# Optimization experiments

Hardware: AMD Instinct MI355X
Metric: run time of the kernel (lower is better)

Reference implementation:

```python
import jax, jax.numpy as jnp
import numpy as np

DEPTH = 2
DIM = 256
MLP = 1024
B = 2
N = 2048


def setup_inputs() -> dict:
    key = jax.random.key(0)
    ks = jax.random.split(key, 6)
    s = 0.02
    d = DIM
    f32 = jnp.float32
    return {
        "x": jax.random.normal(ks[0], (B, N, d), f32),
        "ln1_g": jnp.ones((DEPTH, d), f32),
        "ln1_b": jnp.zeros((DEPTH, d), f32),
        "Wqkv": (jax.random.normal(ks[1], (DEPTH, d, 3 * d), f32) * s),
        "bqkv": jnp.zeros((DEPTH, 3 * d), f32),
        "Wo": (jax.random.normal(ks[2], (DEPTH, d, d), f32) * s),
        "bo": jnp.zeros((DEPTH, d), f32),
        "ln2_g": jnp.ones((DEPTH, d), f32),
        "ln2_b": jnp.zeros((DEPTH, d), f32),
        "W1": (jax.random.normal(ks[3], (DEPTH, d, MLP), f32) * s),
        "b1": jnp.zeros((DEPTH, MLP), f32),
        "W2": (jax.random.normal(ks[4], (DEPTH, MLP, d), f32) * s),
        "b2": jnp.zeros((DEPTH, d), f32),
        "heads": 8,
    }


def _ln(x, g, b, eps=1e-5):
    m = x.mean(-1, keepdims=True)
    v = ((x - m) ** 2).mean(-1, keepdims=True)
    return (x - m) * jax.lax.rsqrt(v + eps) * g + b


def reference(x, ln1_g, ln1_b, Wqkv, bqkv, Wo, bo, ln2_g, ln2_b, W1, b1, W2, b2, heads):
    b, n, dim = x.shape
    hd = dim // heads
    scale = hd ** -0.5
    depth = Wqkv.shape[0]
    out = x
    # NOTE: faithful to original: `x` is never updated inside the loop,
    # so only the last layer's output is returned.
    for i in range(depth):
        y = _ln(x, ln1_g[i], ln1_b[i])
        qkv = y @ Wqkv[i] + bqkv[i]                      # [b,n,3*dim]
        qkv = qkv.reshape(b, n, 3, heads, hd)
        q, k, v = jnp.moveaxis(qkv, 2, 0)                # each [b,n,h,hd]
        q = q.transpose(0, 2, 1, 3)                      # [b,h,n,hd]
        k = k.transpose(0, 2, 1, 3)
        v = v.transpose(0, 2, 1, 3)
        dots = jnp.einsum('bhid,bhjd->bhij', q, k) * scale
        attn = jax.nn.softmax(dots, axis=-1)
        o = jnp.einsum('bhij,bhjd->bhid', attn, v)       # [b,h,n,hd]
        o = o.transpose(0, 2, 1, 3).reshape(b, n, dim)
        o = o @ Wo[i] + bo[i]
        a = o + x                                        # attn residual
        z = _ln(a, ln2_g[i], ln2_b[i])
        m = jax.nn.gelu(z @ W1[i] + b1[i], approximate=False) @ W2[i] + b2[i]
        out = m + a                                      # mlp residual
    return out
```

## Files before the change

kernel.cpp:

```cpp
#include <hip/hip_runtime.h>
#include <hip/hip_bf16.h>
#include <math.h>

#define DEPTHC 2
#define DIMD   256
#define MLPD   1024
#define BB     2
#define NN     2048
#define HH     8
#define HD     32
#define ROWS   (BB * NN)

typedef __attribute__((ext_vector_type(8))) short bf16x8;
typedef __attribute__((ext_vector_type(4))) float f32x4;

__device__ __forceinline__ short f2bf(float x) {
    union { float f; unsigned u; } c; c.f = x;
    unsigned u = c.u + (0x7fffu + ((c.u >> 16) & 1u));
    return (short)(u >> 16);
}
__device__ __forceinline__ float bf2f(short s) {
    union { unsigned u; float f; } c; c.u = ((unsigned)(unsigned short)s) << 16;
    return c.f;
}

__global__ __launch_bounds__(256) void prep(
    const float* __restrict__ Wqkv, const float* __restrict__ Wo,
    const float* __restrict__ W1,   const float* __restrict__ W2,
    short* __restrict__ WqkvF, short* __restrict__ WoF,
    short* __restrict__ W1F,   short* __restrict__ W2F,
    const float* __restrict__ x, const float* __restrict__ g,
    const float* __restrict__ be, short* __restrict__ y)
{
    __shared__ short Ts[128][72];

    if (blockIdx.x >= 96) {
        const int wave = threadIdx.x >> 6;
        const int lane = threadIdx.x & 63;
        const int row  = (blockIdx.x - 96) * 4 + wave;
        const int c    = lane * 4;

        const float4 v = *(const float4*)&x[(size_t)row * DIMD + c];
        float s  = v.x + v.y + v.z + v.w;
        float sq = v.x * v.x + v.y * v.y + v.z * v.z + v.w * v.w;
#pragma unroll
        for (int off = 32; off > 0; off >>= 1) {
            s  += __shfl_down(s,  off, 64);
            sq += __shfl_down(sq, off, 64);
        }
        s  = __shfl(s,  0, 64);
        sq = __shfl(sq, 0, 64);

        const float mean = s * (1.f / DIMD);
        const float var  = sq * (1.f / DIMD) - mean * mean;
        const float rstd = rsqrtf(var + 1e-5f);

        const float4 gg = *(const float4*)&g[c];
        const float4 bb = *(const float4*)&be[c];
        short4 ov;
        ov.x = f2bf((v.x - mean) * rstd * gg.x + bb.x);
        ov.y = f2bf((v.y - mean) * rstd * gg.y + bb.y);
        ov.z = f2bf((v.z - mean) * rstd * gg.z + bb.z);
        ov.w = f2bf((v.w - mean) * rstd * gg.w + bb.w);
        *(short4*)&y[(size_t)row * DIMD + c] = ov;
        return;
    }

    int blk = blockIdx.x;
    const float* W; short* WF; int K, N;
    if (blk < 24)      {           W = Wqkv; WF = WqkvF; K = 256;  N = 768;  }
    else if (blk < 32) { blk -= 24; W = Wo;   WF = WoF;   K = 256;  N = 256;  }
    else if (blk < 64) { blk -= 32; W = W1;   WF = W1F;   K = 256;  N = 1024; }
    else               { blk -= 64; W = W2;   WF = W2F;   K = 1024; N = 256;  }
    const int nkc = K >> 7;
    const int bx  = blk / nkc;
    const int kc  = blk % nkc;
    const int n0  = bx * 64;
    const int k0  = kc * 128;

    const int nc  = threadIdx.x & 63;
    const int kr0 = threadIdx.x >> 6;
#pragma unroll
    for (int i = 0; i < 32; ++i) {
        const int kr = kr0 + i * 4;
        Ts[kr][nc] = f2bf(W[(size_t)(k0 + kr) * N + n0 + nc]);
    }
    __syncthreads();

    short* out = WF + ((size_t)bx * nkc + kc) * 8192;
#pragma unroll
    for (int i = 0; i < 4; ++i) {
        const int u    = threadIdx.x + i * 256;
        const int l16  = u & 15;
        const int quad = (u >> 4) & 3;
        const int nt   = (u >> 6) & 3;
        const int ks   = (u >> 8) & 3;
        const int n    = nt * 16 + l16;
        const int kk   = (ks * 4 + quad) * 8;
        bf16x8 v;
#pragma unroll
        for (int j = 0; j < 8; ++j) v[j] = Ts[kk + j][n];
        *(bf16x8*)&out[(size_t)u * 8] = v;
    }
}

template <int K, bool GELU, bool RES, bool OBF, bool VTG>
__global__ __launch_bounds__(256) void gemm_ks(
    const short* __restrict__ A, const short* __restrict__ WF,
    const float* __restrict__ bias, const float* __restrict__ R,
    void* __restrict__ Cv, int N, short* __restrict__ vtg)
{
    __shared__ short smem[4][4096];

    const int tid  = threadIdx.x;
    const int w    = tid >> 6;
    const int lane = tid & 63;
    const int quad = lane >> 4;
    const int l16  = lane & 15;
    const int n0   = blockIdx.x * 64;
    const int m0   = blockIdx.y * 64;
    constexpr int NKC   = K / 128;
    constexpr int SLICE = K / 4;
    constexpr int NHC   = SLICE / 64;

    const short* wfb  = WF + (size_t)blockIdx.x * NKC * 8192;
    const short* arow = A + (size_t)(m0 + l16) * K + quad * 8;
    short* reg = smem[w];

    f32x4 acc[4][4] = {};

#pragma unroll
    for (int hc = 0; hc < NHC; ++hc) {
        const int kbase = w * SLICE + hc * 64;
        const short* src = wfb +
            ((size_t)(kbase >> 7) * 1024 + (size_t)((kbase >> 6) & 1) * 512) * 8;
#pragma unroll
        for (int i = 0; i < 8; ++i)
            *(bf16x8*)&reg[(i * 64 + lane) * 8] =
                *(const bf16x8*)&src[(size_t)(i * 64 + lane) * 8];

#pragma unroll
        for (int ksl = 0; ksl < 2; ++ksl) {
            const int kk = kbase + ksl * 32;
            bf16x8 af[4];
#pragma unroll
            for (int mt = 0; mt < 4; ++mt)
                af[mt] = *(const bf16x8*)(arow + (size_t)mt * 16 * K + kk);
#pragma unroll
            for (int nt = 0; nt < 4; ++nt) {
                const bf16x8 bf = *(const bf16x8*)
                    &reg[(((ksl * 4 + nt) * 4 + quad) * 16 + l16) * 8];
#pragma unroll
                for (int mt = 0; mt < 4; ++mt)
                    acc[mt][nt] = __builtin_amdgcn_mfma_f32_16x16x32_bf16(
                        af[mt], bf, acc[mt][nt], 0, 0, 0);
            }
        }
    }

#pragma unroll
    for (int p = 0; p < 2; ++p) {
        __syncthreads();
#pragma unroll
        for (int mtl = 0; mtl < 2; ++mtl)
#pragma unroll
            for (int nt = 0; nt < 4; ++nt)
                *(f32x4*)&smem[w][((mtl * 4 + nt) * 64 + lane) * 8] = acc[2 * p + mtl][nt];
        __syncthreads();
        if ((w >> 1) == p) {
            const int mtl = w & 1;
            const int mt  = 2 * p + mtl;
#pragma unroll
            for (int nt = 0; nt < 4; ++nt) {
                const int idx = ((mtl * 4 + nt) * 64 + lane) * 8;
                const f32x4 s0 = *(const f32x4*)&smem[0][idx];
                const f32x4 s1 = *(const f32x4*)&smem[1][idx];
                const f32x4 s2 = *(const f32x4*)&smem[2][idx];
                const f32x4 s3 = *(const f32x4*)&smem[3][idx];
                const f32x4 s  = (s0 + s1) + (s2 + s3);
                const int col  = n0 + nt * 16 + l16;
                const float bb = bias[col];
#pragma unroll
                for (int r = 0; r < 4; ++r) {
                    const int row = m0 + mt * 16 + quad * 4 + r;
                    float v = s[r] + bb;
                    if (RES)  v += R[(size_t)row * N + col];
                    if (GELU) v = 0.5f * v * (1.f + erff(v * 0.70710678118f));
                    const short bv = f2bf(v);
                    if (OBF) ((short*)Cv)[(size_t)row * N + col] = bv;
                    else     ((float*)Cv)[(size_t)row * N + col] = v;
                    if (VTG && n0 >= 2 * DIMD) {
                        const int vc = col - 2 * DIMD;
                        const int b  = row >> 11;
                        const int q  = row & (NN - 1);
                        const int h  = vc >> 5;
                        const int d  = vc & 31;
                        vtg[((size_t)(b * HH + h) * HD + d) * NN + q] = bv;
                    }
                }
            }
        }
    }
}

__global__ __launch_bounds__(256) void ln_kernel(
    const float* __restrict__ x, const float* __restrict__ g,
    const float* __restrict__ bta, short* __restrict__ y)
{
    const int wave = threadIdx.x >> 6;
    const int lane = threadIdx.x & 63;
    const int row  = blockIdx.x * 4 + wave;
    const int c    = lane * 4;

    const float4 v = *(const float4*)&x[(size_t)row * DIMD + c];
    float s  = v.x + v.y + v.z + v.w;
    float sq = v.x * v.x + v.y * v.y + v.z * v.z + v.w * v.w;
#pragma unroll
    for (int off = 32; off > 0; off >>= 1) {
        s  += __shfl_down(s,  off, 64);
        sq += __shfl_down(sq, off, 64);
    }
    s  = __shfl(s,  0, 64);
    sq = __shfl(sq, 0, 64);

    const float mean = s * (1.f / DIMD);
    const float var  = sq * (1.f / DIMD) - mean * mean;
    const float rstd = rsqrtf(var + 1e-5f);

    const float4 gg = *(const float4*)&g[c];
    const float4 bb = *(const float4*)&bta[c];
    short4 ov;
    ov.x = f2bf((v.x - mean) * rstd * gg.x + bb.x);
    ov.y = f2bf((v.y - mean) * rstd * gg.y + bb.y);
    ov.z = f2bf((v.z - mean) * rstd * gg.z + bb.z);
    ov.w = f2bf((v.w - mean) * rstd * gg.w + bb.w);
    *(short4*)&y[(size_t)row * DIMD + c] = ov;
}

__global__ __launch_bounds__(256) void attn_mfma(
    const short* __restrict__ qkv, const short* __restrict__ vtg,
    short* __restrict__ o)
{
    __shared__ __align__(16) short Ks2[2][64][40];
    __shared__ __align__(16) short Vs2[2][32][72];
    __shared__ __align__(16) short Ps[4][16][72];

    const int tid  = threadIdx.x;
    const int w    = tid >> 6;
    const int lane = tid & 63;
    const int quad = lane >> 4;
    const int l16  = lane & 15;
    const int qw    = w & 1;
    const int kside = w >> 1;
    const int bh   = blockIdx.y;
    const int b    = bh >> 3;
    const int h    = bh & 7;
    const int q0   = blockIdx.x * 32 + qw * 16;

    const float scale = 0.17677669529663689f;
    const float shift = 11.090354888959125f;
    const short* base = qkv + (size_t)b * NN * (3 * DIMD);

    const bf16x8 qfrag =
        *(const bf16x8*)(base + (size_t)(q0 + l16) * (3 * DIMD) + h * HD + quad * 8);

    const int side = tid >> 7;
    const int st   = tid & 127;
    const int kr   = st >> 1;
    const int kd   = (st & 1) * 16;
    const int vd   = st >> 2;
    const int vk0  = (st & 3) * 16;

    const short* kgp = base + (size_t)(side * 1024 + kr) * (3 * DIMD)
                       + DIMD + h * HD + kd;
    const short* vgp = vtg + ((size_t)bh * HD + vd) * NN + side * 1024 + vk0;

    f32x4 oacc0 = {0.f, 0.f, 0.f, 0.f};
    f32x4 oacc1 = {0.f, 0.f, 0.f, 0.f};
    float rowsum = 0.f;

    bf16x8 kr0 = *(const bf16x8*)kgp;
    bf16x8 kr1 = *(const bf16x8*)(kgp + 8);
    bf16x8 vr0 = *(const bf16x8*)vgp;
    bf16x8 vr1 = *(const bf16x8*)(vgp + 8);

#pragma unroll 1
    for (int t = 0; t < NN / 128; ++t) {
        __syncthreads();
        *(bf16x8*)&Ks2[side][kr][kd]     = kr0;
        *(bf16x8*)&Ks2[side][kr][kd + 8] = kr1;
        *(bf16x8*)&Vs2[side][vd][vk0]     = vr0;
        *(bf16x8*)&Vs2[side][vd][vk0 + 8] = vr1;
        __syncthreads();

        if (t + 1 < NN / 128) {
            const short* kn = kgp + (size_t)(t + 1) * 64 * (3 * DIMD);
            const short* vn = vgp + (t + 1) * 64;
            kr0 = *(const bf16x8*)kn;
            kr1 = *(const bf16x8*)(kn + 8);
            vr0 = *(const bf16x8*)vn;
            vr1 = *(const bf16x8*)(vn + 8);
        }

        f32x4 s[4];
#pragma unroll
        for (int kt = 0; kt < 4; ++kt) {
            const bf16x8 kf = *(const bf16x8*)&Ks2[kside][kt * 16 + l16][quad * 8];
            f32x4 z = {0.f, 0.f, 0.f, 0.f};
            s[kt] = __builtin_amdgcn_mfma_f32_16x16x32_bf16(kf, qfrag, z, 0, 0, 0);
        }

#pragma unroll
        for (int kt = 0; kt < 4; ++kt) {
            short4 pv;
#pragma unroll
            for (int r = 0; r < 4; ++r) {
                const float p = __expf(fmaf(s[kt][r], scale, -shift));
                rowsum += p;
                union { float f; unsigned u; } cv; cv.f = p;
                ((short*)&pv)[r] = (short)(cv.u >> 16);
            }
            *(short4*)&Ps[w][l16][kt * 16 + quad * 4] = pv;
        }

#pragma unroll
        for (int c = 0; c < 2; ++c) {
            const bf16x8 pf = *(const bf16x8*)&Ps[w][l16][c * 32 + quad * 8];
            const bf16x8 v0 = *(const bf16x8*)&Vs2[kside][l16][c * 32 + quad * 8];
            const bf16x8 v1 = *(const bf16x8*)&Vs2[kside][16 + l16][c * 32 + quad * 8];
            oacc0 = __builtin_amdgcn_mfma_f32_16x16x32_bf16(pf, v0, oacc0, 0, 0, 0);
            oacc1 = __builtin_amdgcn_mfma_f32_16x16x32_bf16(pf, v1, oacc1, 0, 0, 0);
        }
    }

    rowsum += __shfl_xor(rowsum, 16, 64);
    rowsum += __shfl_xor(rowsum, 32, 64);

    float* sc = (float*)&Ks2[0][0][0];
    __syncthreads();
    if (kside == 1) {
        float* o8 = sc + (size_t)(qw * 64 + lane) * 8;
        *(f32x4*)o8       = oacc0;
        *(f32x4*)(o8 + 4) = oacc1;
        if (lane < 16) sc[1024 + qw * 16 + lane] = rowsum;
    }
    __syncthreads();
    if (kside == 0) {
        const float* o8 = sc + (size_t)(qw * 64 + lane) * 8;
        oacc0 += *(const f32x4*)o8;
        oacc1 += *(const f32x4*)(o8 + 4);
        rowsum += sc[1024 + qw * 16 + l16];

#pragma unroll
        for (int r = 0; r < 4; ++r) {
            const float L   = __shfl(rowsum, quad * 4 + r, 16);
            const float inv = 1.f / L;
            const size_t row = (size_t)(b * NN + q0 + quad * 4 + r);
            o[row * DIMD + h * HD + l16]      = f2bf(oacc0[r] * inv);
            o[row * DIMD + h * HD + 16 + l16] = f2bf(oacc1[r] * inv);
        }
    }
}

extern "C" void kernel_launch(void* const* d_in, const int* in_sizes, int n_in,
                              void* d_out, int out_size, void* d_ws, size_t ws_size,
                              hipStream_t stream)
{
    const int L = DEPTHC - 1;
    const float* x     = (const float*)d_in[0];
    const float* ln1_g = (const float*)d_in[1]  + L * DIMD;
    const float* ln1_b = (const float*)d_in[2]  + L * DIMD;
    const float* Wqkv  = (const float*)d_in[3]  + (size_t)L * DIMD * 3 * DIMD;
    const float* bqkv  = (const float*)d_in[4]  + L * 3 * DIMD;
    const float* Wo    = (const float*)d_in[5]  + (size_t)L * DIMD * DIMD;
    const float* bo    = (const float*)d_in[6]  + L * DIMD;
    const float* ln2_g = (const float*)d_in[7]  + L * DIMD;
    const float* ln2_b = (const float*)d_in[8]  + L * DIMD;
    const float* W1    = (const float*)d_in[9]  + (size_t)L * DIMD * MLPD;
    const float* b1    = (const float*)d_in[10] + L * MLPD;
    const float* W2    = (const float*)d_in[11] + (size_t)L * MLPD * DIMD;
    const float* b2    = (const float*)d_in[12] + L * DIMD;
    float* out = (float*)d_out;

    short* WqkvF = (short*)d_ws;
    short* WoF   = WqkvF + 12 * 2 * 8192;
    short* W1F   = WoF   + 4 * 2 * 8192;
    short* W2F   = W1F   + 16 * 2 * 8192;
    short* ybf   = W2F   + 4 * 8 * 8192;
    short* zbf   = ybf   + (size_t)ROWS * DIMD;
    short* qkvbf = zbf   + (size_t)ROWS * DIMD;
    short* vtg   = qkvbf + (size_t)ROWS * 3 * DIMD;
    short* obf   = vtg   + (size_t)16 * HD * NN;
    short* m1bf  = obf   + (size_t)ROWS * DIMD;
    float* a     = (float*)(m1bf + (size_t)ROWS * MLPD);

    prep<<<96 + ROWS / 4, 256, 0, stream>>>(
        Wqkv, Wo, W1, W2, WqkvF, WoF, W1F, W2F, x, ln1_g, ln1_b, ybf);

    gemm_ks<256, false, false, true, true><<<dim3(12, 64), 256, 0, stream>>>(
        ybf, WqkvF, bqkv, nullptr, qkvbf, 3 * DIMD, vtg);

    attn_mfma<<<dim3(NN / 32, BB * HH), 256, 0, stream>>>(qkvbf, vtg, obf);

    gemm_ks<256, false, true, false, false><<<dim3(4, 64), 256, 0, stream>>>(
        obf, WoF, bo, x, a, DIMD, nullptr);

    ln_kernel<<<ROWS / 4, 256, 0, stream>>>(a, ln2_g, ln2_b, zbf);

    gemm_ks<256, true, false, true, false><<<dim3(16, 64), 256, 0, stream>>>(
        zbf, W1F, b1, nullptr, m1bf, MLPD, nullptr);

    gemm_ks<1024, false, true, false, false><<<dim3(4, 64), 256, 0, stream>>>(
        m1bf, W2F, b2, a, out, DIMD, nullptr);
}
```

Measured before the change: 162.5 us.

## Fuse out-projection, LayerNorm2 and MLP into one per-row-tile kernel

Replaces four launches (Wo GEMM, LN2, W1 GEMM with GELU, W2 GEMM) with a single kernel. Each block takes 16 rows and keeps the residual, the normalized activations and the 1024-wide hidden tile in shared memory, so the intermediates never go through global memory. The weights are read straight from global/L2 by every block with no LDS staging, which raises redundant weight traffic. Only 256 blocks run, and each wave keeps a 16-accumulator tile for the W1 stage, which risks low parallelism and register pressure.

```diff
diff --git a/kernel.cpp b/kernel.cpp
--- a/kernel.cpp
+++ b/kernel.cpp
@@ -203,40 +203,6 @@
     }
 }
 
-__global__ __launch_bounds__(256) void ln_kernel(
-    const float* __restrict__ x, const float* __restrict__ g,
-    const float* __restrict__ bta, short* __restrict__ y)
-{
-    const int wave = threadIdx.x >> 6;
-    const int lane = threadIdx.x & 63;
-    const int row  = blockIdx.x * 4 + wave;
-    const int c    = lane * 4;
-
-    const float4 v = *(const float4*)&x[(size_t)row * DIMD + c];
-    float s  = v.x + v.y + v.z + v.w;
-    float sq = v.x * v.x + v.y * v.y + v.z * v.z + v.w * v.w;
-#pragma unroll
-    for (int off = 32; off > 0; off >>= 1) {
-        s  += __shfl_down(s,  off, 64);
-        sq += __shfl_down(sq, off, 64);
-    }
-    s  = __shfl(s,  0, 64);
-    sq = __shfl(sq, 0, 64);
-
-    const float mean = s * (1.f / DIMD);
-    const float var  = sq * (1.f / DIMD) - mean * mean;
-    const float rstd = rsqrtf(var + 1e-5f);
-
-    const float4 gg = *(const float4*)&g[c];
-    const float4 bb = *(const float4*)&bta[c];
-    short4 ov;
-    ov.x = f2bf((v.x - mean) * rstd * gg.x + bb.x);
-    ov.y = f2bf((v.y - mean) * rstd * gg.y + bb.y);
-    ov.z = f2bf((v.z - mean) * rstd * gg.z + bb.z);
-    ov.w = f2bf((v.w - mean) * rstd * gg.w + bb.w);
-    *(short4*)&y[(size_t)row * DIMD + c] = ov;
-}
-
 __global__ __launch_bounds__(256) void attn_mfma(
     const short* __restrict__ qkv, const short* __restrict__ vtg,
     short* __restrict__ o)
@@ -358,6 +324,134 @@
             const size_t row = (size_t)(b * NN + q0 + quad * 4 + r);
             o[row * DIMD + h * HD + l16]      = f2bf(oacc0[r] * inv);
             o[row * DIMD + h * HD + 16 + l16] = f2bf(oacc1[r] * inv);
+        }
+    }
+}
+
+__global__ __launch_bounds__(256) void tail_fused(
+    const short* __restrict__ obf, const float* __restrict__ x,
+    const short* __restrict__ WoF, const float* __restrict__ bo,
+    const float* __restrict__ ln2g, const float* __restrict__ ln2b,
+    const short* __restrict__ W1F, const float* __restrict__ b1,
+    const short* __restrict__ W2F, const float* __restrict__ b2,
+    float* __restrict__ out)
+{
+    __shared__ __align__(16) float aS[16][260];
+    __shared__ __align__(16) short zS[16][264];
+    __shared__ __align__(16) short mS[16][1032];
+
+    const int tid  = threadIdx.x;
+    const int w    = tid >> 6;
+    const int lane = tid & 63;
+    const int quad = lane >> 4;
+    const int l16  = lane & 15;
+    const int m0   = blockIdx.x * 16;
+
+    {
+        const short* arow   = obf + (size_t)(m0 + l16) * DIMD + quad * 8;
+        const short* wchunk = WoF + (size_t)w * 2 * 8192;
+        f32x4 acc[4] = {};
+#pragma unroll
+        for (int ks = 0; ks < 8; ++ks) {
+            const int k = ks * 32;
+            const bf16x8 af = *(const bf16x8*)(arow + k);
+            const int ub = (k >> 7) * 1024 + ((k >> 5) & 3) * 256 + quad * 16 + l16;
+#pragma unroll
+            for (int nt = 0; nt < 4; ++nt) {
+                const bf16x8 bf = *(const bf16x8*)&wchunk[(size_t)(ub + nt * 64) * 8];
+                acc[nt] = __builtin_amdgcn_mfma_f32_16x16x32_bf16(af, bf, acc[nt], 0, 0, 0);
+            }
+        }
+#pragma unroll
+        for (int nt = 0; nt < 4; ++nt) {
+            const int col  = w * 64 + nt * 16 + l16;
+            const float bb = bo[col];
+#pragma unroll
+            for (int r = 0; r < 4; ++r) {
+                const int row = quad * 4 + r;
+                aS[row][col] = acc[nt][r] + bb + x[(size_t)(m0 + row) * DIMD + col];
+            }
+        }
+    }
+    __syncthreads();
+
+    {
+        const int row = tid >> 4;
+        const int seg = (tid & 15) * 16;
+        float s = 0.f, sq = 0.f;
+#pragma unroll
+        for (int i = 0; i < 16; ++i) {
+            const float v = aS[row][seg + i];
+            s += v; sq += v * v;
+        }
+#pragma unroll
+        for (int off = 1; off < 16; off <<= 1) {
+            s  += __shfl_xor(s,  off, 64);
+            sq += __shfl_xor(sq, off, 64);
+        }
+        const float mean = s * (1.f / DIMD);
+        const float var  = sq * (1.f / DIMD) - mean * mean;
+        const float rstd = rsqrtf(var + 1e-5f);
+#pragma unroll
+        for (int i = 0; i < 16; ++i) {
+            const int c = seg + i;
+            zS[row][c] = f2bf((aS[row][c] - mean) * rstd * ln2g[c] + ln2b[c]);
+        }
+    }
+    __syncthreads();
+
+    {
+        f32x4 acc[16] = {};
+#pragma unroll
+        for (int ks = 0; ks < 8; ++ks) {
+            const int k = ks * 32;
+            const bf16x8 af = *(const bf16x8*)&zS[l16][k + quad * 8];
+            const int ub = (k >> 7) * 1024 + ((k >> 5) & 3) * 256 + quad * 16 + l16;
+#pragma unroll
+            for (int nt = 0; nt < 16; ++nt) {
+                const int bx = w * 4 + (nt >> 2);
+                const bf16x8 bf = *(const bf16x8*)
+                    &W1F[(size_t)bx * 2 * 8192 + (size_t)(ub + (nt & 3) * 64) * 8];
+                acc[nt] = __builtin_amdgcn_mfma_f32_16x16x32_bf16(af, bf, acc[nt], 0, 0, 0);
+            }
+        }
+#pragma unroll
+        for (int nt = 0; nt < 16; ++nt) {
+            const int col  = w * 256 + nt * 16 + l16;
+            const float bb = b1[col];
+#pragma unroll
+            for (int r = 0; r < 4; ++r) {
+                float v = acc[nt][r] + bb;
+                v = 0.5f * v * (1.f + erff(v * 0.70710678118f));
+                mS[quad * 4 + r][col] = f2bf(v);
+            }
+        }
+    }
+    __syncthreads();
+
+    {
+        f32x4 acc[4] = {};
+        const short* wchunk = W2F + (size_t)w * 8 * 8192;
+#pragma unroll
+        for (int ks = 0; ks < 32; ++ks) {
+            const int k = ks * 32;
+            const bf16x8 af = *(const bf16x8*)&mS[l16][k + quad * 8];
+            const int ub = (k >> 7) * 1024 + ((k >> 5) & 3) * 256 + quad * 16 + l16;
+#pragma unroll
+            for (int nt = 0; nt < 4; ++nt) {
+                const bf16x8 bf = *(const bf16x8*)&wchunk[(size_t)(ub + nt * 64) * 8];
+                acc[nt] = __builtin_amdgcn_mfma_f32_16x16x32_bf16(af, bf, acc[nt], 0, 0, 0);
+            }
+        }
+#pragma unroll
+        for (int nt = 0; nt < 4; ++nt) {
+            const int col  = w * 64 + nt * 16 + l16;
+            const float bb = b2[col];
+#pragma unroll
+            for (int r = 0; r < 4; ++r) {
+                const int row = quad * 4 + r;
+                out[(size_t)(m0 + row) * DIMD + col] = acc[nt][r] + bb + aS[row][col];
+            }
         }
     }
 }
@@ -387,12 +481,9 @@
     short* W1F   = WoF   + 4 * 2 * 8192;
     short* W2F   = W1F   + 16 * 2 * 8192;
     short* ybf   = W2F   + 4 * 8 * 8192;
-    short* zbf   = ybf   + (size_t)ROWS * DIMD;
-    short* qkvbf = zbf   + (size_t)ROWS * DIMD;
+    short* qkvbf = ybf   + (size_t)ROWS * DIMD;
     short* vtg   = qkvbf + (size_t)ROWS * 3 * DIMD;
     short* obf   = vtg   + (size_t)16 * HD * NN;
-    short* m1bf  = obf   + (size_t)ROWS * DIMD;
-    float* a     = (float*)(m1bf + (size_t)ROWS * MLPD);
 
     prep<<<96 + ROWS / 4, 256, 0, stream>>>(
         Wqkv, Wo, W1, W2, WqkvF, WoF, W1F, W2F, x, ln1_g, ln1_b, ybf);
@@ -402,14 +493,6 @@
 
     attn_mfma<<<dim3(NN / 32, BB * HH), 256, 0, stream>>>(qkvbf, vtg, obf);
 
-    gemm_ks<256, false, true, false, false><<<dim3(4, 64), 256, 0, stream>>>(
-        obf, WoF, bo, x, a, DIMD, nullptr);
-
-    ln_kernel<<<ROWS / 4, 256, 0, stream>>>(a, ln2_g, ln2_b, zbf);
-
-    gemm_ks<256, true, false, true, false><<<dim3(16, 64), 256, 0, stream>>>(
-        zbf, W1F, b1, nullptr, m1bf, MLPD, nullptr);
-
-    gemm_ks<1024, false, true, false, false><<<dim3(4, 64), 256, 0, stream>>>(
-        m1bf, W2F, b2, a, out, DIMD, nullptr);
-}
+    tail_fused<<<ROWS / 16, 256, 0, stream>>>(
+        obf, x, WoF, bo, ln2_g, ln2_b, W1F, b1, W2F, b2, out);
+}
```

Result: faster. 157.8 us (-2.9%).
